# Performance work log

Measured on AMD Instinct MI355X. Metric: run time of the kernel, lower is better.

## Reference

```python
import jax, jax.numpy as jnp
from jax import lax
import numpy as np

B, N = 2, 1024  # batch of NxN linear-system matrices
DN = ('NCHW', 'OIHW', 'NCHW')


def _conv(x, w, b, pad):
    # cross-correlation, same convention as torch/spconv
    return lax.conv_general_dilated(x, w, (1, 1), pad, dimension_numbers=DN) + b[None, :, None, None]


def _spread_mask(m, pad):
    # regular sparse conv: output site active iff any input site in 2x2 window is active
    ones = jnp.ones((1, 1, 2, 2), dtype=m.dtype)
    return (lax.conv_general_dilated(m, ones, (1, 1), pad, dimension_numbers=DN) > 0).astype(m.dtype)


def _prelu(x, a):
    return jnp.where(x >= 0, x, a * x)


def setup_inputs() -> dict:
    key = jax.random.key(0)
    ks = jax.random.split(key, 10)
    mask = jax.random.randint(ks[0], (B, N, N), 0, 2, dtype=jnp.int32)
    x = jax.random.normal(ks[1], (B, 1, N, N), dtype=jnp.float32)

    def w(k, o, i, kh, kw):
        return jax.random.normal(k, (o, i, kh, kw), dtype=jnp.float32) / np.sqrt(i * kh * kw)

    def bias(k, o):
        return 0.01 * jax.random.normal(k, (o,), dtype=jnp.float32)

    return {
        'x': x, 'mask': mask,
        'w1': w(ks[2], 8, 1, 1, 1), 'b1': bias(ks[6], 8), 'a1': jnp.float32(0.25),
        'w2': w(ks[3], 16, 8, 2, 2), 'b2': bias(ks[7], 16), 'a2': jnp.float32(0.25),
        'w3': w(ks[4], 8, 16, 2, 2), 'b3': bias(ks[8], 8), 'a3': jnp.float32(0.25),
        'w4': w(ks[5], 1, 8, 1, 1), 'b4': bias(ks[9], 1),
    }


def reference(x, mask, w1, b1, a1, w2, b2, a2, w3, b3, a3, w4, b4):
    m = (mask > 0).astype(jnp.float32)[:, None]          # [B,1,N,N] active-site mask
    h = x * m                                            # sparse input: zeros at inactive sites
    # layer 1: 1x1 conv + PReLU (mask unchanged)
    h = _conv(h, w1, b1, ((0, 0), (0, 0))) * m
    h = _prelu(h, a1)
    # layer 2: 2x2 conv, padding (1,0) -> [B,16,N+1,N-1]
    p2 = ((1, 1), (0, 0))
    m2 = _spread_mask(m, p2)
    h = _conv(h, w2, b2, p2) * m2
    h = _prelu(h, a2)
    # layer 3: 2x2 conv, padding (0,1) -> [B,8,N,N]
    p3 = ((0, 0), (1, 1))
    m3 = _spread_mask(m2, p3)
    h = _conv(h, w3, b3, p3) * m3
    h = _prelu(h, a3)
    # layer 4: 1x1 conv (mask unchanged)
    h = _conv(h, w4, b4, ((0, 0), (0, 0))) * m3          # [B,1,N,N]
    # triangular masking on sparse indices (row=indices[:,1], col=indices[:,2])
    row = jnp.arange(N)[:, None]
    col = jnp.arange(N)[None, :]
    h = jnp.where((row >= col)[None, None], h, jnp.float32(0))
    diag_active = (row == col)[None, None] & (m3 > 0)
    h = jnp.where(diag_active, jax.nn.softplus(h), h)
    return h
```

## Files before the change

### kernel.cpp

```cpp
#include <hip/hip_runtime.h>
#include <hip/hip_bf16.h>
#include <math.h>

#define N 1024
#define TB 16

typedef __attribute__((ext_vector_type(8))) short short8;
typedef __attribute__((ext_vector_type(4))) short short4v;
typedef __attribute__((ext_vector_type(4))) float f32x4;

__device__ __forceinline__ float prelu(float v, float a) {
    return fmaxf(v, 0.f) + a * fminf(v, 0.f);
}

__device__ __forceinline__ short f2bf(float f) {
    return (short)__bfloat16_as_ushort(__float2bfloat16(f));
}

__global__ __launch_bounds__(256, 8) void precond_mfma(
    const float* __restrict__ xg, const int* __restrict__ maskg,
    const float* __restrict__ w1, const float* __restrict__ b1, const float* __restrict__ a1p,
    const float* __restrict__ w2, const float* __restrict__ b2, const float* __restrict__ a2p,
    const float* __restrict__ w3, const float* __restrict__ b3, const float* __restrict__ a3p,
    const float* __restrict__ w4, const float* __restrict__ b4p,
    float* __restrict__ out)
{
    const int tid = threadIdx.x;
    const int bz  = blockIdx.z;
    const int t   = blockIdx.x;

    int by = (int)((sqrtf(8.0f * (float)t + 1.0f) - 1.0f) * 0.5f);
    while ((by + 1) * (by + 2) / 2 <= t) ++by;
    while (by * (by + 1) / 2 > t) --by;
    const int bx = t - by * (by + 1) / 2;
    const int ty0 = by * TB, tx0 = bx * TB;

    if (t < 2016) {
        int y = (int)((sqrtf(8.0f * (float)t + 1.0f) + 1.0f) * 0.5f);
        while (y * (y - 1) / 2 > t) --y;
        while ((y + 1) * y / 2 <= t) ++y;
        int xs = t - y * (y - 1) / 2;
        int zy = xs * TB + (tid >> 4), zx = y * TB + (tid & 15);
        out[((size_t)bz * N + zy) * N + zx] = 0.f;
    }

    __shared__ __align__(16) short sW2[512];
    __shared__ __align__(16) short sW3[1024];
    __shared__ __align__(16) short h1s[324 * 8];
    __shared__ __align__(16) short h2lo[289 * 8];
    __shared__ __align__(16) short h2hi[289 * 8];
    __shared__ __align__(16) unsigned RM1[12];
    __shared__ __align__(16) unsigned M2f[10];

    const int lane = tid & 63, wid = tid >> 6;
    const int c16 = lane & 15, g = lane >> 4;

    const float a1 = a1p[0], a2 = a2p[0], a3 = a3p[0];
    const float b4 = b4p[0];
    const bool leftEdge  = (tx0 == 0);
    const bool rightEdge = (tx0 == N - TB);

    for (int u = tid; u < 512; u += 256) {
        int o = u >> 5, khkw = (u >> 3) & 3, i = u & 7;
        sW2[u] = f2bf(w2[((o * 8 + i) * 2 + (khkw >> 1)) * 2 + (khkw & 1)]);
    }
    for (int u = tid; u < 1024; u += 256) {
        int oc = u >> 6, k = u & 63, khkw = k >> 4, i = k & 15;
        sW3[u] = (oc < 8) ? f2bf(w3[((oc * 16 + i) * 2 + (khkw >> 1)) * 2 + (khkw & 1)]) : (short)0;
    }

    for (int p = tid; p < 324; p += 256) {
        int dy = p / 18, dx = p - dy * 18;
        int gy = ty0 - 1 + dy, gx = tx0 - 1 + dx;
        bool mb = false;
        float xv = 0.f;
        if ((unsigned)gy < N && (unsigned)gx < N) {
            size_t idx = ((size_t)bz * N + gy) * N + gx;
            mb = (maskg[idx] > 0);
            xv = xg[idx];
        }
        unsigned long long bal = __ballot(mb);
        if (lane == 0) {
            int c = (p - lane) >> 6;
            *(uint2*)&RM1[2 * c] = make_uint2((unsigned)bal, (unsigned)(bal >> 32));
        }
        short8 hv;
#pragma unroll
        for (int ch = 0; ch < 8; ++ch) hv[ch] = f2bf(prelu(fmaf(xv, w1[ch], b1[ch]), a1));
        if (!mb) hv = (short8)0;
        *(short8*)&h1s[p * 8] = hv;
    }
    __syncthreads();

    {
        short8 a2f = *(const short8*)&sW2[c16 * 32 + g * 8];
        const int kh = g >> 1, kw = g & 1;
        f32x4 bias2;
#pragma unroll
        for (int r = 0; r < 4; ++r) bias2[r] = b2[g * 4 + r];

#pragma unroll
        for (int k = 0; k < 5; ++k) {
            if (k == 4 && wid == 3) break;
            const int grp = (k < 4) ? (wid + 4 * k) : (16 + wid);
            int p = grp * 16 + c16;
            bool valid = p < 289;
            int pc = valid ? p : 288;
            int dy2 = pc / 17, dx2 = pc - dy2 * 17;

            short8 bf = *(const short8*)&h1s[((dy2 + kh) * 18 + dx2 + kw) * 8];
            f32x4 acc = __builtin_amdgcn_mfma_f32_16x16x32_bf16(a2f, bf, bias2, 0, 0, 0);

            int q = dy2 * 18 + dx2, w0 = q >> 5, sh = q & 31;
            unsigned long long v64 = ((unsigned long long)RM1[w0 + 1] << 32) | RM1[w0];
            unsigned long long v = v64 >> sh;
            unsigned m2 = (unsigned)((v | (v >> 1) | (v >> 18) | (v >> 19)) & 1ull);
            if ((leftEdge && dx2 == 0) || (rightEdge && dx2 == 16)) m2 = 0;
            if (!valid) m2 = 0;

            unsigned long long balm = __ballot(m2 != 0);
            if (lane == 0) ((unsigned short*)M2f)[grp] = (unsigned short)(balm & 0xFFFFull);

            short4v hv;
#pragma unroll
            for (int r = 0; r < 4; ++r) hv[r] = f2bf(prelu(acc[r], a2));
            if (m2 == 0) { hv[0] = 0; hv[1] = 0; hv[2] = 0; hv[3] = 0; }

            if (valid) {
                short* dst = (g & 2) ? (short*)h2hi : (short*)h2lo;
                *(short4v*)&dst[pc * 8 + (g & 1) * 4] = hv;
            }
        }
    }
    __syncthreads();

    {
        short8 a3f0 = *(const short8*)&sW3[c16 * 64 + g * 8];
        short8 a3f1 = *(const short8*)&sW3[c16 * 64 + 32 + g * 8];
        const int kw = g >> 1, ic8 = g & 1;
        const short* h2sel = ic8 ? (const short*)h2hi : (const short*)h2lo;
        const int base = wid * 4;
        f32x4 bias3;
        float w4r[4];
#pragma unroll
        for (int r = 0; r < 4; ++r) {
            bias3[r] = (g < 2) ? b3[g * 4 + r] : 0.f;
            w4r[r]   = (g < 2) ? w4[g * 4 + r] : 0.f;
        }

        short8 bfp = *(const short8*)&h2sel[(base * 17 + c16 + kw) * 8];
#pragma unroll
        for (int j = 0; j < 4; ++j) {
            const int G = base + j;
            short8 bfn = *(const short8*)&h2sel[((G + 1) * 17 + c16 + kw) * 8];
            f32x4 acc = __builtin_amdgcn_mfma_f32_16x16x32_bf16(a3f0, bfp, bias3, 0, 0, 0);
            acc = __builtin_amdgcn_mfma_f32_16x16x32_bf16(a3f1, bfn, acc, 0, 0, 0);
            bfp = bfn;

            float partial = 0.f;
#pragma unroll
            for (int r = 0; r < 4; ++r) partial = fmaf(prelu(acc[r], a3), w4r[r], partial);
            partial += __shfl_xor(partial, 16, 64);

            if (g == 0) {
                int q2 = G * 17 + c16, w2i = q2 >> 5, sh2 = q2 & 31;
                unsigned long long v64 = ((unsigned long long)M2f[w2i + 1] << 32) | M2f[w2i];
                unsigned long long v = v64 >> sh2;
                unsigned m3 = (unsigned)((v | (v >> 1) | (v >> 17) | (v >> 18)) & 1ull);

                float outv = m3 ? (partial + b4) : 0.f;
                int y = ty0 + G, x = tx0 + c16;
                if (y < x) {
                    outv = 0.f;
                } else if (y == x && m3) {
                    outv = fmaxf(outv, 0.f) + log1pf(expf(-fabsf(outv)));
                }
                out[((size_t)bz * N + y) * N + x] = outv;
            }
        }
    }
}

extern "C" void kernel_launch(void* const* d_in, const int* in_sizes, int n_in,
                              void* d_out, int out_size, void* d_ws, size_t ws_size,
                              hipStream_t stream) {
    const float* x    = (const float*)d_in[0];
    const int*   mask = (const int*)  d_in[1];
    const float* w1   = (const float*)d_in[2];
    const float* b1   = (const float*)d_in[3];
    const float* a1   = (const float*)d_in[4];
    const float* w2   = (const float*)d_in[5];
    const float* b2   = (const float*)d_in[6];
    const float* a2   = (const float*)d_in[7];
    const float* w3   = (const float*)d_in[8];
    const float* b3   = (const float*)d_in[9];
    const float* a3   = (const float*)d_in[10];
    const float* w4   = (const float*)d_in[11];
    const float* b4   = (const float*)d_in[12];
    float* out = (float*)d_out;

    dim3 grid(2080, 1, 2);
    precond_mfma<<<grid, 256, 0, stream>>>(x, mask, w1, b1, a1, w2, b2, a2,
                                           w3, b3, a3, w4, b4, out);
}
```

Before: 27.56 us.

## Process both batch images per block and prefetch second batch inputs

Each block now handles both batch elements in sequence instead of launching a separate z-slice per batch. The global loads of mask and x for the second batch are issued before the first batch's layer-3 compute, so load latency overlaps with MFMA work. Weight fragments, biases and tile-index math are computed once and reused. This halves the grid size and adds register pressure plus a serial dependency within each block, which may reduce latency hiding across blocks.

```diff
diff --git a/kernel.cpp b/kernel.cpp
--- a/kernel.cpp
+++ b/kernel.cpp
@@ -26,7 +26,6 @@
     float* __restrict__ out)
 {
     const int tid = threadIdx.x;
-    const int bz  = blockIdx.z;
     const int t   = blockIdx.x;
 
     int by = (int)((sqrtf(8.0f * (float)t + 1.0f) - 1.0f) * 0.5f);
@@ -40,8 +39,9 @@
         while (y * (y - 1) / 2 > t) --y;
         while ((y + 1) * y / 2 <= t) ++y;
         int xs = t - y * (y - 1) / 2;
-        int zy = xs * TB + (tid >> 4), zx = y * TB + (tid & 15);
-        out[((size_t)bz * N + zy) * N + zx] = 0.f;
+        size_t o0 = ((size_t)(xs * TB + (tid >> 4))) * N + y * TB + (tid & 15);
+        out[o0] = 0.f;
+        out[o0 + (size_t)N * N] = 0.f;
     }
 
     __shared__ __align__(16) short sW2[512];
@@ -69,36 +69,58 @@
         sW3[u] = (oc < 8) ? f2bf(w3[((oc * 16 + i) * 2 + (khkw >> 1)) * 2 + (khkw & 1)]) : (short)0;
     }
 
-    for (int p = tid; p < 324; p += 256) {
-        int dy = p / 18, dx = p - dy * 18;
-        int gy = ty0 - 1 + dy, gx = tx0 - 1 + dx;
-        bool mb = false;
-        float xv = 0.f;
+    const int pA0 = tid;
+    const int pA1 = tid + 256;
+    const bool s1valid = (pA1 < 324);
+    const bool s1wave  = ((tid - lane) + 256 < 324);
+
+    const int dyA0 = pA0 / 18, dxA0 = pA0 - dyA0 * 18;
+    const int dyA1 = pA1 / 18, dxA1 = pA1 - dyA1 * 18;
+
+    {
+        int gy = ty0 - 1 + dyA0, gx = tx0 - 1 + dxA0;
+        bool mb = false; float xv = 0.f;
         if ((unsigned)gy < N && (unsigned)gx < N) {
-            size_t idx = ((size_t)bz * N + gy) * N + gx;
-            mb = (maskg[idx] > 0);
-            xv = xg[idx];
+            size_t idx = ((size_t)gy) * N + gx;
+            mb = (maskg[idx] > 0); xv = xg[idx];
         }
         unsigned long long bal = __ballot(mb);
-        if (lane == 0) {
-            int c = (p - lane) >> 6;
-            *(uint2*)&RM1[2 * c] = make_uint2((unsigned)bal, (unsigned)(bal >> 32));
-        }
+        if (lane == 0) *(uint2*)&RM1[2 * wid] = make_uint2((unsigned)bal, (unsigned)(bal >> 32));
         short8 hv;
 #pragma unroll
         for (int ch = 0; ch < 8; ++ch) hv[ch] = f2bf(prelu(fmaf(xv, w1[ch], b1[ch]), a1));
         if (!mb) hv = (short8)0;
-        *(short8*)&h1s[p * 8] = hv;
+        *(short8*)&h1s[pA0 * 8] = hv;
+
+        if (s1wave) {
+            bool mb1 = false; float xv1 = 0.f;
+            if (s1valid) {
+                int gy1 = ty0 - 1 + dyA1, gx1 = tx0 - 1 + dxA1;
+                if ((unsigned)gy1 < N && (unsigned)gx1 < N) {
+                    size_t idx = ((size_t)gy1) * N + gx1;
+                    mb1 = (maskg[idx] > 0); xv1 = xg[idx];
+                }
+            }
+            unsigned long long bal1 = __ballot(mb1);
+            if (lane == 0) *(uint2*)&RM1[2 * (wid + 4)] = make_uint2((unsigned)bal1, (unsigned)(bal1 >> 32));
+            if (s1valid) {
+                short8 hv1;
+#pragma unroll
+                for (int ch = 0; ch < 8; ++ch) hv1[ch] = f2bf(prelu(fmaf(xv1, w1[ch], b1[ch]), a1));
+                if (!mb1) hv1 = (short8)0;
+                *(short8*)&h1s[pA1 * 8] = hv1;
+            }
+        }
     }
     __syncthreads();
 
-    {
-        short8 a2f = *(const short8*)&sW2[c16 * 32 + g * 8];
+    short8 a2f = *(const short8*)&sW2[c16 * 32 + g * 8];
+    f32x4 bias2;
+#pragma unroll
+    for (int r = 0; r < 4; ++r) bias2[r] = b2[g * 4 + r];
+
+    {
         const int kh = g >> 1, kw = g & 1;
-        f32x4 bias2;
-#pragma unroll
-        for (int r = 0; r < 4; ++r) bias2[r] = b2[g * 4 + r];
-
 #pragma unroll
         for (int k = 0; k < 5; ++k) {
             if (k == 4 && wid == 3) break;
@@ -134,25 +156,42 @@
     }
     __syncthreads();
 
-    {
-        short8 a3f0 = *(const short8*)&sW3[c16 * 64 + g * 8];
-        short8 a3f1 = *(const short8*)&sW3[c16 * 64 + 32 + g * 8];
-        const int kw = g >> 1, ic8 = g & 1;
-        const short* h2sel = ic8 ? (const short*)h2hi : (const short*)h2lo;
-        const int base = wid * 4;
-        f32x4 bias3;
-        float w4r[4];
-#pragma unroll
-        for (int r = 0; r < 4; ++r) {
-            bias3[r] = (g < 2) ? b3[g * 4 + r] : 0.f;
-            w4r[r]   = (g < 2) ? w4[g * 4 + r] : 0.f;
-        }
-
-        short8 bfp = *(const short8*)&h2sel[(base * 17 + c16 + kw) * 8];
+    bool mbZ0 = false, mbZ1 = false;
+    float xvZ0 = 0.f, xvZ1 = 0.f;
+    {
+        int gy = ty0 - 1 + dyA0, gx = tx0 - 1 + dxA0;
+        if ((unsigned)gy < N && (unsigned)gx < N) {
+            size_t idx = (size_t)N * N + (size_t)gy * N + gx;
+            mbZ0 = (maskg[idx] > 0); xvZ0 = xg[idx];
+        }
+        if (s1valid) {
+            int gy1 = ty0 - 1 + dyA1, gx1 = tx0 - 1 + dxA1;
+            if ((unsigned)gy1 < N && (unsigned)gx1 < N) {
+                size_t idx = (size_t)N * N + (size_t)gy1 * N + gx1;
+                mbZ1 = (maskg[idx] > 0); xvZ1 = xg[idx];
+            }
+        }
+    }
+
+    short8 a3f0 = *(const short8*)&sW3[c16 * 64 + g * 8];
+    short8 a3f1 = *(const short8*)&sW3[c16 * 64 + 32 + g * 8];
+    const int kwC = g >> 1, ic8 = g & 1;
+    const short* h2sel = ic8 ? (const short*)h2hi : (const short*)h2lo;
+    const int base = wid * 4;
+    f32x4 bias3;
+    float w4r[4];
+#pragma unroll
+    for (int r = 0; r < 4; ++r) {
+        bias3[r] = (g < 2) ? b3[g * 4 + r] : 0.f;
+        w4r[r]   = (g < 2) ? w4[g * 4 + r] : 0.f;
+    }
+
+    {
+        short8 bfp = *(const short8*)&h2sel[(base * 17 + c16 + kwC) * 8];
 #pragma unroll
         for (int j = 0; j < 4; ++j) {
             const int G = base + j;
-            short8 bfn = *(const short8*)&h2sel[((G + 1) * 17 + c16 + kw) * 8];
+            short8 bfn = *(const short8*)&h2sel[((G + 1) * 17 + c16 + kwC) * 8];
             f32x4 acc = __builtin_amdgcn_mfma_f32_16x16x32_bf16(a3f0, bfp, bias3, 0, 0, 0);
             acc = __builtin_amdgcn_mfma_f32_16x16x32_bf16(a3f1, bfn, acc, 0, 0, 0);
             bfp = bfn;
@@ -175,7 +214,100 @@
                 } else if (y == x && m3) {
                     outv = fmaxf(outv, 0.f) + log1pf(expf(-fabsf(outv)));
                 }
-                out[((size_t)bz * N + y) * N + x] = outv;
+                out[((size_t)y) * N + x] = outv;
+            }
+        }
+    }
+
+    {
+        unsigned long long bal = __ballot(mbZ0);
+        if (lane == 0) *(uint2*)&RM1[2 * wid] = make_uint2((unsigned)bal, (unsigned)(bal >> 32));
+        short8 hv;
+#pragma unroll
+        for (int ch = 0; ch < 8; ++ch) hv[ch] = f2bf(prelu(fmaf(xvZ0, w1[ch], b1[ch]), a1));
+        if (!mbZ0) hv = (short8)0;
+        *(short8*)&h1s[pA0 * 8] = hv;
+
+        if (s1wave) {
+            unsigned long long bal1 = __ballot(mbZ1);
+            if (lane == 0) *(uint2*)&RM1[2 * (wid + 4)] = make_uint2((unsigned)bal1, (unsigned)(bal1 >> 32));
+            if (s1valid) {
+                short8 hv1;
+#pragma unroll
+                for (int ch = 0; ch < 8; ++ch) hv1[ch] = f2bf(prelu(fmaf(xvZ1, w1[ch], b1[ch]), a1));
+                if (!mbZ1) hv1 = (short8)0;
+                *(short8*)&h1s[pA1 * 8] = hv1;
+            }
+        }
+    }
+    __syncthreads();
+
+    {
+        const int kh = g >> 1, kw = g & 1;
+#pragma unroll
+        for (int k = 0; k < 5; ++k) {
+            if (k == 4 && wid == 3) break;
+            const int grp = (k < 4) ? (wid + 4 * k) : (16 + wid);
+            int p = grp * 16 + c16;
+            bool valid = p < 289;
+            int pc = valid ? p : 288;
+            int dy2 = pc / 17, dx2 = pc - dy2 * 17;
+
+            short8 bf = *(const short8*)&h1s[((dy2 + kh) * 18 + dx2 + kw) * 8];
+            f32x4 acc = __builtin_amdgcn_mfma_f32_16x16x32_bf16(a2f, bf, bias2, 0, 0, 0);
+
+            int q = dy2 * 18 + dx2, w0 = q >> 5, sh = q & 31;
+            unsigned long long v64 = ((unsigned long long)RM1[w0 + 1] << 32) | RM1[w0];
+            unsigned long long v = v64 >> sh;
+            unsigned m2 = (unsigned)((v | (v >> 1) | (v >> 18) | (v >> 19)) & 1ull);
+            if ((leftEdge && dx2 == 0) || (rightEdge && dx2 == 16)) m2 = 0;
+            if (!valid) m2 = 0;
+
+            unsigned long long balm = __ballot(m2 != 0);
+            if (lane == 0) ((unsigned short*)M2f)[grp] = (unsigned short)(balm & 0xFFFFull);
+
+            short4v hv;
+#pragma unroll
+            for (int r = 0; r < 4; ++r) hv[r] = f2bf(prelu(acc[r], a2));
+            if (m2 == 0) { hv[0] = 0; hv[1] = 0; hv[2] = 0; hv[3] = 0; }
+
+            if (valid) {
+                short* dst = (g & 2) ? (short*)h2hi : (short*)h2lo;
+                *(short4v*)&dst[pc * 8 + (g & 1) * 4] = hv;
+            }
+        }
+    }
+    __syncthreads();
+
+    {
+        short8 bfp = *(const short8*)&h2sel[(base * 17 + c16 + kwC) * 8];
+#pragma unroll
+        for (int j = 0; j < 4; ++j) {
+            const int G = base + j;
+            short8 bfn = *(const short8*)&h2sel[((G + 1) * 17 + c16 + kwC) * 8];
+            f32x4 acc = __builtin_amdgcn_mfma_f32_16x16x32_bf16(a3f0, bfp, bias3, 0, 0, 0);
+            acc = __builtin_amdgcn_mfma_f32_16x16x32_bf16(a3f1, bfn, acc, 0, 0, 0);
+            bfp = bfn;
+
+            float partial = 0.f;
+#pragma unroll
+            for (int r = 0; r < 4; ++r) partial = fmaf(prelu(acc[r], a3), w4r[r], partial);
+            partial += __shfl_xor(partial, 16, 64);
+
+            if (g == 0) {
+                int q2 = G * 17 + c16, w2i = q2 >> 5, sh2 = q2 & 31;
+                unsigned long long v64 = ((unsigned long long)M2f[w2i + 1] << 32) | M2f[w2i];
+                unsigned long long v = v64 >> sh2;
+                unsigned m3 = (unsigned)((v | (v >> 1) | (v >> 17) | (v >> 18)) & 1ull);
+
+                float outv = m3 ? (partial + b4) : 0.f;
+                int y = ty0 + G, x = tx0 + c16;
+                if (y < x) {
+                    outv = 0.f;
+                } else if (y == x && m3) {
+                    outv = fmaxf(outv, 0.f) + log1pf(expf(-fabsf(outv)));
+                }
+                out[(size_t)N * N + (size_t)y * N + x] = outv;
             }
         }
     }
@@ -199,7 +331,7 @@
     const float* b4   = (const float*)d_in[12];
     float* out = (float*)d_out;
 
-    dim3 grid(2080, 1, 2);
+    dim3 grid(2080, 1, 1);
     precond_mfma<<<grid, 256, 0, stream>>>(x, mask, w1, b1, a1, w2, b2, a2,
                                            w3, b3, a3, w4, b4, out);
 }
```

Result: slower. 41.09 us (+49.1%).

## Give each wave a private layer-2 halo to drop the inter-layer barrier

Applied to the files above, without the earlier changes.

Each wave now computes its own five rows of layer-2 activations (its four output rows plus one halo row) into a per-wave LDS slice, instead of the block sharing one 17x17 tile. That removes the __syncthreads between layers 2 and 3. The layer-2 activity mask now lives in registers as three 32-bit words, replacing the shared M2f array, and the layer-3 mask is taken with simple bit shifts. In exchange, layer-2 MFMA work and LDS footprint grow because halo rows are computed twice by adjacent waves.

```diff
diff --git a/kernel.cpp b/kernel.cpp
--- a/kernel.cpp
+++ b/kernel.cpp
@@ -47,10 +47,9 @@
     __shared__ __align__(16) short sW2[512];
     __shared__ __align__(16) short sW3[1024];
     __shared__ __align__(16) short h1s[324 * 8];
-    __shared__ __align__(16) short h2lo[289 * 8];
-    __shared__ __align__(16) short h2hi[289 * 8];
+    __shared__ __align__(16) short h2lo[4][85 * 8];
+    __shared__ __align__(16) short h2hi[4][85 * 8];
     __shared__ __align__(16) unsigned RM1[12];
-    __shared__ __align__(16) unsigned M2f[10];
 
     const int lane = tid & 63, wid = tid >> 6;
     const int c16 = lane & 15, g = lane >> 4;
@@ -92,21 +91,23 @@
     }
     __syncthreads();
 
+    unsigned M2w0, M2w1, M2w2;
     {
         short8 a2f = *(const short8*)&sW2[c16 * 32 + g * 8];
         const int kh = g >> 1, kw = g & 1;
+        const int rowbase = wid * 4;
         f32x4 bias2;
 #pragma unroll
         for (int r = 0; r < 4; ++r) bias2[r] = b2[g * 4 + r];
 
-#pragma unroll
-        for (int k = 0; k < 5; ++k) {
-            if (k == 4 && wid == 3) break;
-            const int grp = (k < 4) ? (wid + 4 * k) : (16 + wid);
-            int p = grp * 16 + c16;
-            bool valid = p < 289;
-            int pc = valid ? p : 288;
-            int dy2 = pc / 17, dx2 = pc - dy2 * 17;
+        unsigned mw[3] = {0, 0, 0};
+#pragma unroll
+        for (int grp = 0; grp < 6; ++grp) {
+            int pl = grp * 16 + c16;
+            bool valid = pl < 85;
+            int plc = valid ? pl : 84;
+            int lr = plc / 17, dx2 = plc - lr * 17;
+            int dy2 = rowbase + lr;
 
             short8 bf = *(const short8*)&h1s[((dy2 + kh) * 18 + dx2 + kw) * 8];
             f32x4 acc = __builtin_amdgcn_mfma_f32_16x16x32_bf16(a2f, bf, bias2, 0, 0, 0);
@@ -118,8 +119,13 @@
             if ((leftEdge && dx2 == 0) || (rightEdge && dx2 == 16)) m2 = 0;
             if (!valid) m2 = 0;
 
-            unsigned long long balm = __ballot(m2 != 0);
-            if (lane == 0) ((unsigned short*)M2f)[grp] = (unsigned short)(balm & 0xFFFFull);
+            unsigned bits16 = (unsigned)(__ballot(m2 != 0) & 0xFFFFull);
+            if (grp == 0) mw[0]  = bits16;
+            if (grp == 1) mw[0] |= bits16 << 16;
+            if (grp == 2) mw[1]  = bits16;
+            if (grp == 3) mw[1] |= bits16 << 16;
+            if (grp == 4) mw[2]  = bits16;
+            if (grp == 5) mw[2] |= bits16 << 16;
 
             short4v hv;
 #pragma unroll
@@ -127,19 +133,18 @@
             if (m2 == 0) { hv[0] = 0; hv[1] = 0; hv[2] = 0; hv[3] = 0; }
 
             if (valid) {
-                short* dst = (g & 2) ? (short*)h2hi : (short*)h2lo;
-                *(short4v*)&dst[pc * 8 + (g & 1) * 4] = hv;
+                short* dst = (g & 2) ? &h2hi[wid][0] : &h2lo[wid][0];
+                *(short4v*)&dst[plc * 8 + (g & 1) * 4] = hv;
             }
         }
-    }
-    __syncthreads();
+        M2w0 = mw[0]; M2w1 = mw[1]; M2w2 = mw[2];
+    }
 
     {
         short8 a3f0 = *(const short8*)&sW3[c16 * 64 + g * 8];
         short8 a3f1 = *(const short8*)&sW3[c16 * 64 + 32 + g * 8];
-        const int kw = g >> 1, ic8 = g & 1;
-        const short* h2sel = ic8 ? (const short*)h2hi : (const short*)h2lo;
-        const int base = wid * 4;
+        const int kwC = g >> 1, ic8 = g & 1;
+        const short* h2sel = ic8 ? &h2hi[wid][0] : &h2lo[wid][0];
         f32x4 bias3;
         float w4r[4];
 #pragma unroll
@@ -148,11 +153,17 @@
             w4r[r]   = (g < 2) ? w4[g * 4 + r] : 0.f;
         }
 
-        short8 bfp = *(const short8*)&h2sel[(base * 17 + c16 + kw) * 8];
+        unsigned rm[5];
+        rm[0] = M2w0 & 0x1FFFFu;
+        rm[1] = (unsigned)((((unsigned long long)M2w1 << 32) | M2w0) >> 17) & 0x1FFFFu;
+        rm[2] = (M2w1 >> 2) & 0x1FFFFu;
+        rm[3] = (unsigned)((((unsigned long long)M2w2 << 32) | M2w1) >> 19) & 0x1FFFFu;
+        rm[4] = (M2w2 >> 4) & 0x1FFFFu;
+
+        short8 bfp = *(const short8*)&h2sel[(c16 + kwC) * 8];
 #pragma unroll
         for (int j = 0; j < 4; ++j) {
-            const int G = base + j;
-            short8 bfn = *(const short8*)&h2sel[((G + 1) * 17 + c16 + kw) * 8];
+            short8 bfn = *(const short8*)&h2sel[((j + 1) * 17 + c16 + kwC) * 8];
             f32x4 acc = __builtin_amdgcn_mfma_f32_16x16x32_bf16(a3f0, bfp, bias3, 0, 0, 0);
             acc = __builtin_amdgcn_mfma_f32_16x16x32_bf16(a3f1, bfn, acc, 0, 0, 0);
             bfp = bfn;
@@ -163,13 +174,11 @@
             partial += __shfl_xor(partial, 16, 64);
 
             if (g == 0) {
-                int q2 = G * 17 + c16, w2i = q2 >> 5, sh2 = q2 & 31;
-                unsigned long long v64 = ((unsigned long long)M2f[w2i + 1] << 32) | M2f[w2i];
-                unsigned long long v = v64 >> sh2;
-                unsigned m3 = (unsigned)((v | (v >> 1) | (v >> 17) | (v >> 18)) & 1ull);
+                unsigned combined = rm[j] | rm[j + 1];
+                unsigned m3 = (combined >> c16) & 3u;
 
                 float outv = m3 ? (partial + b4) : 0.f;
-                int y = ty0 + G, x = tx0 + c16;
+                int y = ty0 + wid * 4 + j, x = tx0 + c16;
                 if (y < x) {
                     outv = 0.f;
                 } else if (y == x && m3) {
```

Measured after the change: 27.16 us. Within noise of the previous version (-1.4%).
